# Performance work log

Hardware: AMD Instinct MI355X
Metric: run time of the kernel (lower is better)

The kernel has to match this reference:

```python
import jax, jax.numpy as jnp
import numpy as np

N = 50000      # nodes
E = 500000     # edges
D = 128        # in_dim == out_dim
L = 4          # encoder_layers
G = 64         # graphs in batch
FIXED = 10000  # fixed_input_dim
BN_EPS = 1e-5


def setup_inputs() -> dict:
    key = jax.random.key(0)
    ks = jax.random.split(key, 14)
    s = 0.05
    feat_id = jax.random.randint(ks[0], (N,), 0, FIXED)
    edge_index = jax.random.randint(ks[1], (2, E), 0, N)
    # sorted graph assignment guaranteeing all G graphs are non-empty
    batch = (jnp.arange(N) * G) // N
    return {
        "feat_id": feat_id,
        "edge_index": edge_index,
        "batch": batch,
        # value_projection: Linear(FIXED, D); store weight.T as a lookup table
        "value_proj_w": jax.random.normal(ks[2], (FIXED, D)) * s,
        "value_proj_b": jax.random.normal(ks[3], (D,)) * s,
        "deg_emb": jax.random.normal(ks[4], (1001, D)) * s,
        # stacked per-layer GIN MLP params: Linear -> BN -> ReLU -> Linear
        "mlp_w1": jax.random.normal(ks[5], (L, D, D)) * s,
        "mlp_b1": jax.random.normal(ks[6], (L, D)) * s,
        "bn1_g": 1.0 + 0.1 * jax.random.normal(ks[7], (L, D)),
        "bn1_b": 0.1 * jax.random.normal(ks[8], (L, D)),
        "mlp_w2": jax.random.normal(ks[9], (L, D, D)) * s,
        "mlp_b2": jax.random.normal(ks[10], (L, D)) * s,
        # outer per-layer BatchNorm1d
        "bn2_g": 1.0 + 0.1 * jax.random.normal(ks[11], (L, D)),
        "bn2_b": 0.1 * jax.random.normal(ks[12], (L, D)),
    }


def _bn(x, g, b):
    # BatchNorm1d in training mode: batch stats over the node axis, biased var
    mu = jnp.mean(x, axis=0)
    var = jnp.mean(jnp.square(x - mu), axis=0)
    return g * (x - mu) * jax.lax.rsqrt(var + BN_EPS) + b


def reference(feat_id, edge_index, batch, value_proj_w, value_proj_b, deg_emb,
              mlp_w1, mlp_b1, bn1_g, bn1_b, mlp_w2, mlp_b2, bn2_g, bn2_b):
    src, dst = edge_index[0], edge_index[1]
    # one_hot(feat_id % FIXED) @ W.T + b  ==  gather of transposed weight rows
    h_attr = value_proj_w[feat_id % FIXED] + value_proj_b  # [N, D]
    # in-degree embedding (clamped to [0, 1000])
    in_deg = jax.ops.segment_sum(jnp.ones((E,), jnp.int32), dst, num_segments=N)
    h = h_attr + deg_emb[jnp.clip(in_deg, 0, 1000)]
    for i in range(L):
        # GIN: sum_{j in N(v)} h_j + (1 + eps) * h_v, eps = 0 (learn_eps=False)
        agg = jax.ops.segment_sum(h[src], dst, num_segments=N) + h
        z = jax.nn.relu(_bn(agg @ mlp_w1[i] + mlp_b1[i], bn1_g[i], bn1_b[i]))
        z = z @ mlp_w2[i] + mlp_b2[i]
        h = jax.nn.relu(_bn(z, bn2_g[i], bn2_b[i]))
    # global mean pool per graph
    gsum = jax.ops.segment_sum(h, batch, num_segments=G)       # [G, D]
    cnt = jax.ops.segment_sum(jnp.ones((N, 1)), batch, num_segments=G)
    graph_feature = gsum / jnp.maximum(cnt, 1.0)
    return graph_feature, h
```

## Files before the change

### kernel.cpp

```cpp
#include <hip/hip_runtime.h>

#define NN 50000
#define NE 500000
#define DD 128
#define NL 4
#define NG 64
#define FIXED_DIM 10000
#define BN_EPS 1e-5f
#define NB 196

typedef unsigned short u16;
typedef unsigned int u32;
typedef __attribute__((ext_vector_type(8))) short bf16x8;
typedef __attribute__((ext_vector_type(4))) float f32x4;

__device__ __forceinline__ float bf2f(u16 u) {
    return __uint_as_float(((u32)u) << 16);
}
__device__ __forceinline__ u16 f2bf(float f) {
    u32 u = __float_as_uint(f);
    return (u16)((u + 0x7FFFu + ((u >> 16) & 1u)) >> 16);
}
__device__ __forceinline__ float ldf(const void* p, size_t i, int isbf) {
    return isbf ? bf2f(((const u16*)p)[i]) : ((const float*)p)[i];
}

__global__ void k_pre(const void* __restrict__ vb, int* __restrict__ flag,
                      const int* __restrict__ batch, int* __restrict__ goff,
                      float* __restrict__ zbase, int zwords) {
    int b = blockIdx.x, t = threadIdx.x;
    if (b == 0) {
        __shared__ int ok[256];
        float v = (t < 128) ? bf2f(((const u16*)vb)[t]) : 0.f;
        ok[t] = (t < 128) ? ((fabsf(v) < 1000.f) ? 1 : 0) : 1;
        __syncthreads();
        for (int off = 128; off; off >>= 1) {
            if (t < off) ok[t] &= ok[t + off];
            __syncthreads();
        }
        if (t == 0) *flag = ok[0];
    } else if (b == 1) {
        if (t <= NG) {
            int lo = 0, hi = NN;
            while (lo < hi) {
                int mid = (lo + hi) >> 1;
                if (batch[mid] < t) lo = mid + 1; else hi = mid;
            }
            goff[t] = lo;
        }
    } else {
        int i = (b - 2) * 256 + t;
        if (i < zwords) zbase[i] = 0.f;
    }
}

__global__ void k_cvtswz(const void* b1, const void* b2, const void* g1,
                         const void* be1, const void* g2, const void* be2,
                         const void* __restrict__ w1, const void* __restrict__ w2,
                         float* __restrict__ pc, u16* __restrict__ Wsw,
                         const int* __restrict__ flag) {
    int b = blockIdx.x, tt = threadIdx.x;
    if (b < 12) {
        int t = b * 256 + tt;
        int p = t >> 9, j = t & 511;
        const void* s = (p == 0) ? b1 : (p == 1) ? b2 : (p == 2) ? g1
                      : (p == 3) ? be1 : (p == 4) ? g2 : be2;
        pc[t] = ldf(s, j, *flag);
    } else {
        int t = (b - 12) * 256 + tt;
        int m    = t >> 14;
        int idx  = t & 16383;
        int nt   = idx >> 11;
        int ks   = (idx >> 9) & 3;
        int lane = (idx >> 3) & 63;
        int j    = idx & 7;
        int row = ks * 32 + (lane >> 4) * 8 + j;
        int col = nt * 16 + (lane & 15);
        const void* src = (m < 4) ? w1 : w2;
        size_t off = (size_t)(m & 3) * DD * DD + (size_t)row * DD + col;
        Wsw[t] = f2bf(ldf(src, off, *flag));
    }
}

__global__ void k_deg(const int* __restrict__ dst, int* __restrict__ deg) {
    int i = blockIdx.x * 256 + threadIdx.x;
    if (i < NE) atomicAdd(&deg[dst[i]], 1);
}

__global__ void k_scan12(const int* __restrict__ deg, int* __restrict__ bsum,
                         int* __restrict__ sem) {
    __shared__ int S[256];
    __shared__ int lastB;
    int b = blockIdx.x, t = threadIdx.x;
    int i = b * 256 + t;
    S[t] = (i < NN) ? deg[i] : 0;
    __syncthreads();
    for (int off = 128; off; off >>= 1) {
        if (t < off) S[t] += S[t + off];
        __syncthreads();
    }
    if (t == 0) {
        atomicExch(&bsum[b], S[0]);
        __threadfence();
        lastB = (atomicAdd(&sem[0], 1) == gridDim.x - 1);
    }
    __syncthreads();
    if (!lastB) return;
    __threadfence();
    int v = (t < NB) ? atomicAdd(&bsum[t], 0) : 0;
    S[t] = v;
    __syncthreads();
    for (int off = 1; off < 256; off <<= 1) {
        int x = (t >= off) ? S[t - off] : 0;
        __syncthreads();
        S[t] += x;
        __syncthreads();
    }
    if (t < NB) bsum[t] = S[t] - v;
}

__global__ void k_scan3init(const int* __restrict__ deg, const int* __restrict__ bsum,
                            int* __restrict__ rowptr,
                            const int* __restrict__ feat, const void* __restrict__ vw,
                            const void* __restrict__ vb, const void* __restrict__ demb,
                            u16* __restrict__ B, const int* __restrict__ flag) {
    __shared__ int S[256];
    int b = blockIdx.x, t = threadIdx.x;
    if (b < NB) {
        int i = b * 256 + t;
        int v = (i < NN) ? deg[i] : 0;
        S[t] = v;
        __syncthreads();
        for (int off = 1; off < 256; off <<= 1) {
            int x = (t >= off) ? S[t - off] : 0;
            __syncthreads();
            S[t] += x;
            __syncthreads();
        }
        if (i < NN) rowptr[i] = bsum[b] + S[t] - v;
        if (i == NN - 1) rowptr[NN] = bsum[b] + S[t];
    } else {
        int idx = (b - NB) * 256 + t;
        if (idx >= NN * DD) return;
        int n = idx >> 7, c = idx & 127;
        int isbf = *flag;
        int f = feat[n] % FIXED_DIM;
        int dg = min(deg[n], 1000);
        B[idx] = f2bf(ldf(vw, (size_t)f * DD + c, isbf)
                    + ldf(vb, c, isbf)
                    + ldf(demb, (size_t)dg * DD + c, isbf));
    }
}

__global__ void k_fill(const int* __restrict__ src, const int* __restrict__ dst,
                       const int* __restrict__ rowptr, int* __restrict__ cursor,
                       int* __restrict__ colidx) {
    int e = blockIdx.x * 256 + threadIdx.x;
    if (e >= NE) return;
    int d = dst[e];
    int p = atomicAdd(&cursor[d], 1);
    colidx[rowptr[d] + p] = src[e];
}

template <bool AFF>
__global__ __launch_bounds__(256, 8) void k_aggr(
        const u16* __restrict__ B, const int* __restrict__ rowptr,
        const int* __restrict__ colidx,
        const float* __restrict__ gIn, const float* __restrict__ bIn,
        const float* __restrict__ sIn, const float* __restrict__ qIn,
        u16* __restrict__ Agg) {
    int n = blockIdx.x * 4 + (threadIdx.x >> 6);
    if (n >= NN) return;
    int c = (threadIdx.x & 63) * 2;
    float a0 = 1.f, b0 = 0.f, a1 = 1.f, b1 = 0.f;
    if (AFF) {
        float inv = 1.0f / (float)NN;
        float mu0 = sIn[c] * inv, mu1 = sIn[c + 1] * inv;
        float v0 = fmaxf(qIn[c] * inv - mu0 * mu0, 0.f);
        float v1 = fmaxf(qIn[c + 1] * inv - mu1 * mu1, 0.f);
        a0 = gIn[c] * rsqrtf(v0 + BN_EPS);
        a1 = gIn[c + 1] * rsqrtf(v1 + BN_EPS);
        b0 = bIn[c] - a0 * mu0;
        b1 = bIn[c + 1] - a1 * mu1;
    }
    u32 w = *(const u32*)&B[(size_t)n * DD + c];
    float x0 = bf2f((u16)(w & 0xFFFF)), x1 = bf2f((u16)(w >> 16));
    float s0 = AFF ? fmaxf(fmaf(a0, x0, b0), 0.f) : x0;
    float s1 = AFF ? fmaxf(fmaf(a1, x1, b1), 0.f) : x1;
    int lo = rowptr[n], hi = rowptr[n + 1];
    int j = lo;
    for (; j + 4 <= hi; j += 4) {
        int m0 = colidx[j], m1 = colidx[j + 1];
        int m2 = colidx[j + 2], m3 = colidx[j + 3];
        u32 w0 = *(const u32*)&B[(size_t)m0 * DD + c];
        u32 w1v = *(const u32*)&B[(size_t)m1 * DD + c];
        u32 w2v = *(const u32*)&B[(size_t)m2 * DD + c];
        u32 w3v = *(const u32*)&B[(size_t)m3 * DD + c];
        float y;
        y = bf2f((u16)(w0 & 0xFFFF)); s0 += AFF ? fmaxf(fmaf(a0, y, b0), 0.f) : y;
        y = bf2f((u16)(w0 >> 16));    s1 += AFF ? fmaxf(fmaf(a1, y, b1), 0.f) : y;
        y = bf2f((u16)(w1v & 0xFFFF)); s0 += AFF ? fmaxf(fmaf(a0, y, b0), 0.f) : y;
        y = bf2f((u16)(w1v >> 16));    s1 += AFF ? fmaxf(fmaf(a1, y, b1), 0.f) : y;
        y = bf2f((u16)(w2v & 0xFFFF)); s0 += AFF ? fmaxf(fmaf(a0, y, b0), 0.f) : y;
        y = bf2f((u16)(w2v >> 16));    s1 += AFF ? fmaxf(fmaf(a1, y, b1), 0.f) : y;
        y = bf2f((u16)(w3v & 0xFFFF)); s0 += AFF ? fmaxf(fmaf(a0, y, b0), 0.f) : y;
        y = bf2f((u16)(w3v >> 16));    s1 += AFF ? fmaxf(fmaf(a1, y, b1), 0.f) : y;
    }
    for (; j < hi; j++) {
        int m = colidx[j];
        w = *(const u32*)&B[(size_t)m * DD + c];
        x0 = bf2f((u16)(w & 0xFFFF)); x1 = bf2f((u16)(w >> 16));
        s0 += AFF ? fmaxf(fmaf(a0, x0, b0), 0.f) : x0;
        s1 += AFF ? fmaxf(fmaf(a1, x1, b1), 0.f) : x1;
    }
    *(u32*)&Agg[(size_t)n * DD + c] = ((u32)f2bf(s1) << 16) | (u32)f2bf(s0);
}

template <bool IN16, bool OUT16, bool AFF>
__global__ __launch_bounds__(256, 2) void k_gemm(
        const void* In, const u16* __restrict__ Wsw,
        const float* __restrict__ bias,
        const float* __restrict__ gIn, const float* __restrict__ bIn,
        const float* __restrict__ sIn, const float* __restrict__ qIn,
        void* Out, float* __restrict__ ssum, float* __restrict__ ssq,
        int nRows) {
    __shared__ u16 Wl[16384];
    __shared__ u16 At[128 * 136];
    __shared__ float affS[256];
    float* RedS = (float*)At;
    float* RedQ = RedS + 512;
    const int t = threadIdx.x;
    const int row0 = blockIdx.x * 128;

    if (AFF) {
        if (t < 128) {
            float inv = 1.0f / (float)NN;
            float mu = sIn[t] * inv;
            float var = fmaxf(qIn[t] * inv - mu * mu, 0.f);
            float a = gIn[t] * rsqrtf(var + BN_EPS);
            affS[t] = a;
            affS[128 + t] = bIn[t] - a * mu;
        }
        __syncthreads();
    }

    {
        const uint4* s = (const uint4*)Wsw;
        uint4* d = (uint4*)Wl;
        #pragma unroll
        for (int i = 0; i < 8; i++) d[t + i * 256] = s[t + i * 256];
    }
    if (IN16) {
        for (int i = t; i < 2048; i += 256) {
            int r  = i >> 4;
            int c8 = (i & 15) * 8;
            int gr = row0 + r;
            uint4 v = make_uint4(0u, 0u, 0u, 0u);
            if (gr < nRows) v = *(const uint4*)&((const u16*)In)[(size_t)gr * DD + c8];
            *(uint4*)&At[r * 136 + c8] = v;
        }
    } else {
        for (int i = t; i < 4096; i += 256) {
            int r  = i >> 5;
            int c4 = (i & 31) * 4;
            int gr = row0 + r;
            float4 v = make_float4(0.f, 0.f, 0.f, 0.f);
            if (gr < nRows) {
                v = *(const float4*)&((const float*)In)[(size_t)gr * DD + c4];
                if (AFF) {
                    v.x = fmaxf(fmaf(affS[c4 + 0], v.x, affS[128 + c4 + 0]), 0.f);
                    v.y = fmaxf(fmaf(affS[c4 + 1], v.y, affS[128 + c4 + 1]), 0.f);
                    v.z = fmaxf(fmaf(affS[c4 + 2], v.z, affS[128 + c4 + 2]), 0.f);
                    v.w = fmaxf(fmaf(affS[c4 + 3], v.w, affS[128 + c4 + 3]), 0.f);
                }
            }
            ushort4 o;
            o.x = f2bf(v.x); o.y = f2bf(v.y); o.z = f2bf(v.z); o.w = f2bf(v.w);
            *(ushort4*)&At[r * 136 + c4] = o;
        }
    }
    __syncthreads();

    const int w    = t >> 6;
    const int ln   = t & 63;
    const int quad = ln >> 4;
    const int lq   = ln & 15;

    f32x4 acc0[8], acc1[8];
    #pragma unroll
    for (int nt = 0; nt < 8; nt++) {
        acc0[nt] = (f32x4){0.f, 0.f, 0.f, 0.f};
        acc1[nt] = (f32x4){0.f, 0.f, 0.f, 0.f};
    }

    const u16* aRow0 = &At[(w * 32 + lq) * 136 + quad * 8];
    const u16* aRow1 = &At[(w * 32 + 16 + lq) * 136 + quad * 8];
    #pragma unroll
    for (int ks = 0; ks < 4; ks++) {
        bf16x8 a0 = *(const bf16x8*)&aRow0[ks * 32];
        bf16x8 a1 = *(const bf16x8*)&aRow1[ks * 32];
        #pragma unroll
        for (int nt = 0; nt < 8; nt++) {
            bf16x8 b = *(const bf16x8*)&Wl[((nt * 4 + ks) * 64 + ln) * 8];
            acc0[nt] = __builtin_amdgcn_mfma_f32_16x16x32_bf16(a0, b, acc0[nt], 0, 0, 0);
            acc1[nt] = __builtin_amdgcn_mfma_f32_16x16x32_bf16(a1, b, acc1[nt], 0, 0, 0);
        }
    }
    __syncthreads();

    const int rb0 = row0 + w * 32 + quad * 4;
    const int rb1 = rb0 + 16;
    #pragma unroll
    for (int nt = 0; nt < 8; nt++) {
        int col = nt * 16 + lq;
        float bv = bias[col];
        float s = 0.f, q = 0.f;
        #pragma unroll
        for (int r = 0; r < 4; r++) {
            int gr = rb0 + r;
            if (gr < nRows) {
                float val = acc0[nt][r] + bv;
                size_t o = (size_t)gr * DD + col;
                if (OUT16) ((u16*)Out)[o] = f2bf(val);
                else       ((float*)Out)[o] = val;
                s += val; q += val * val;
            }
        }
        #pragma unroll
        for (int r = 0; r < 4; r++) {
            int gr = rb1 + r;
            if (gr < nRows) {
                float val = acc1[nt][r] + bv;
                size_t o = (size_t)gr * DD + col;
                if (OUT16) ((u16*)Out)[o] = f2bf(val);
                else       ((float*)Out)[o] = val;
                s += val; q += val * val;
            }
        }
        s += __shfl_xor(s, 16); q += __shfl_xor(q, 16);
        s += __shfl_xor(s, 32); q += __shfl_xor(q, 32);
        if (quad == 0) { RedS[w * 128 + col] = s; RedQ[w * 128 + col] = q; }
    }
    __syncthreads();
    if (t < 128) {
        float s = RedS[t] + RedS[128 + t] + RedS[256 + t] + RedS[384 + t];
        float q = RedQ[t] + RedQ[128 + t] + RedQ[256 + t] + RedQ[384 + t];
        atomicAdd(&ssum[t], s);
        atomicAdd(&ssq[t], q);
    }
}

__global__ __launch_bounds__(256, 4) void k_upool(
        const u16* __restrict__ Bz,
        const float* __restrict__ gIn, const float* __restrict__ bIn,
        const float* __restrict__ sIn, const float* __restrict__ qIn,
        const int* __restrict__ batch, float* __restrict__ A,
        float* __restrict__ gsum, const int* __restrict__ goff,
        float* __restrict__ outw, int* __restrict__ sem) {
    const int t = threadIdx.x;
    const int c = (t & 63) * 2;
    const int qv = t >> 6;
    const int r0 = blockIdx.x * 64;
    const int g_lo = batch[r0];
    const int g_hi = batch[min(r0 + 63, NN - 1)];
    float inv = 1.0f / (float)NN;
    float mu0 = sIn[c] * inv, mu1 = sIn[c + 1] * inv;
    float v0 = fmaxf(qIn[c] * inv - mu0 * mu0, 0.f);
    float v1 = fmaxf(qIn[c + 1] * inv - mu1 * mu1, 0.f);
    float a0 = gIn[c] * rsqrtf(v0 + BN_EPS);
    float a1 = gIn[c + 1] * rsqrtf(v1 + BN_EPS);
    float b0 = bIn[c] - a0 * mu0;
    float b1 = bIn[c + 1] - a1 * mu1;
    float lo0 = 0.f, lo1 = 0.f, hi0 = 0.f, hi1 = 0.f;
    #pragma unroll
    for (int i = 0; i < 16; i++) {
        int r = r0 + qv + 4 * i;
        if (r >= NN) break;
        u32 wd = *(const u32*)&Bz[(size_t)r * DD + c];
        float x0 = fmaxf(fmaf(a0, bf2f((u16)(wd & 0xFFFF)), b0), 0.f);
        float x1 = fmaxf(fmaf(a1, bf2f((u16)(wd >> 16)), b1), 0.f);
        *(float2*)&A[(size_t)r * DD + c] = make_float2(x0, x1);
        if (batch[r] == g_lo) { lo0 += x0; lo1 += x1; }
        else                  { hi0 += x0; hi1 += x1; }
    }
    __shared__ float2 PL[4][64];
    __shared__ float2 PH[4][64];
    PL[qv][t & 63] = make_float2(lo0, lo1);
    PH[qv][t & 63] = make_float2(hi0, hi1);
    __syncthreads();
    if (t < 64) {
        float2 p0 = PL[0][t], p1 = PL[1][t], p2 = PL[2][t], p3 = PL[3][t];
        atomicAdd(&gsum[(size_t)g_lo * DD + 2 * t],     p0.x + p1.x + p2.x + p3.x);
        atomicAdd(&gsum[(size_t)g_lo * DD + 2 * t + 1], p0.y + p1.y + p2.y + p3.y);
    } else if (t < 128 && g_hi != g_lo) {
        int u = t - 64;
        float2 p0 = PH[0][u], p1 = PH[1][u], p2 = PH[2][u], p3 = PH[3][u];
        atomicAdd(&gsum[(size_t)g_hi * DD + 2 * u],     p0.x + p1.x + p2.x + p3.x);
        atomicAdd(&gsum[(size_t)g_hi * DD + 2 * u + 1], p0.y + p1.y + p2.y + p3.y);
    }

    __shared__ int lastF;
    if (t == 0) {
        __threadfence();
        lastF = (atomicAdd(&sem[1], 1) == gridDim.x - 1);
    }
    __syncthreads();
    if (!lastF) return;
    __threadfence();
    for (int i = t; i < NG * DD; i += 256) {
        int g = i >> 7;
        float cnt = fmaxf((float)(goff[g + 1] - goff[g]), 1.0f);
        outw[i] = atomicAdd(&gsum[i], 0.0f) / cnt;
    }
}

extern "C" void kernel_launch(void* const* d_in, const int* in_sizes, int n_in,
                              void* d_out, int out_size, void* d_ws, size_t ws_size,
                              hipStream_t stream) {
    const int* feat  = (const int*)d_in[0];
    const int* ei    = (const int*)d_in[1];
    const int* batch = (const int*)d_in[2];
    const void* vw   = d_in[3];
    const void* vb   = d_in[4];
    const void* demb = d_in[5];
    const void* w1   = d_in[6];
    const void* b1   = d_in[7];
    const void* g1   = d_in[8];
    const void* be1  = d_in[9];
    const void* w2   = d_in[10];
    const void* b2   = d_in[11];
    const void* g2   = d_in[12];
    const void* be2  = d_in[13];

    const int* src = ei;
    const int* dst = ei + NE;
    const size_t ND = (size_t)NN * DD;

    float* pc     = (float*)d_ws;
    int*   flag   = (int*)(pc + 3072);
    float* stats  = (float*)(flag + 64);
    float* gsum   = stats + 2048;
    int*   deg    = (int*)(gsum + 8192);
    int*   cursor = deg + NN;
    int*   sem    = cursor + NN;
    int*   bsum   = sem + 64;
    int*   goff   = bsum + 256;
    int*   rowptr = goff + 128;
    int*   colidx = rowptr + NN + 64;
    u16*   Wsw    = (u16*)(colidx + NE);
    u16*   B      = Wsw + 8 * 16384;
    u16*   Agg16  = B + ND;

    float* b1c  = pc;
    float* b2c  = pc + 512;
    float* g1c  = pc + 1024;
    float* be1c = pc + 1536;
    float* g2c  = pc + 2048;
    float* be2c = pc + 2560;
    float* sum1 = stats;
    float* sq1  = stats + 512;
    float* sum2 = stats + 1024;
    float* sq2  = stats + 1536;

    float* outw = (float*)d_out;
    float* A    = outw + (size_t)NG * DD;

    const int zwords = 2048 + 8192 + NN + NN + 64;
    const int gridND = (int)(ND / 256);
    const int gemmBlocks = (NN + 127) / 128;
    const int aggrBlocks = (NN + 3) / 4;

    k_pre<<<2 + (zwords + 255) / 256, 256, 0, stream>>>(vb, flag, batch, goff,
                                                        stats, zwords);
    k_cvtswz<<<12 + 512, 256, 0, stream>>>(b1, b2, g1, be1, g2, be2, w1, w2,
                                           pc, Wsw, flag);
    k_deg<<<(NE + 255) / 256, 256, 0, stream>>>(dst, deg);
    k_scan12<<<NB, 256, 0, stream>>>(deg, bsum, sem);
    k_scan3init<<<NB + gridND, 256, 0, stream>>>(deg, bsum, rowptr,
                                                 feat, vw, vb, demb, B, flag);
    k_fill<<<(NE + 255) / 256, 256, 0, stream>>>(src, dst, rowptr, cursor, colidx);

    for (int l = 0; l < NL; l++) {
        const u16* W1l = Wsw + (size_t)l * 16384;
        const u16* W2l = Wsw + (size_t)(4 + l) * 16384;
        if (l == 0) {
            k_aggr<false><<<aggrBlocks, 256, 0, stream>>>(
                B, rowptr, colidx, nullptr, nullptr, nullptr, nullptr, Agg16);
        } else {
            k_aggr<true><<<aggrBlocks, 256, 0, stream>>>(
                B, rowptr, colidx, g2c + (l - 1) * 128, be2c + (l - 1) * 128,
                sum2 + (l - 1) * 128, sq2 + (l - 1) * 128, Agg16);
        }
        k_gemm<true, false, false><<<gemmBlocks, 256, 0, stream>>>(
            Agg16, W1l, b1c + l * 128, nullptr, nullptr, nullptr, nullptr,
            A, sum1 + l * 128, sq1 + l * 128, NN);
        k_gemm<false, true, true><<<gemmBlocks, 256, 0, stream>>>(
            A, W2l, b2c + l * 128, g1c + l * 128, be1c + l * 128,
            sum1 + l * 128, sq1 + l * 128,
            B, sum2 + l * 128, sq2 + l * 128, NN);
    }
    k_upool<<<(NN + 63) / 64, 256, 0, stream>>>(
        B, g2c + 3 * 128, be2c + 3 * 128, sum2 + 3 * 128, sq2 + 3 * 128,
        batch, A, gsum, goff, outw, sem);
}
```

Before: 548.4 us.

## Fuse both GIN MLP GEMMs into one kernel with grid barrier for BN stats

Merges the two per-layer GEMM kernels into a single persistent kernel. The first GEMM's output stays in registers, a software grid-wide barrier on a semaphore waits for the global BN1 statistics, then BN+ReLU is applied in place and the second GEMM runs from LDS. This avoids writing and re-reading the fp32 intermediate activation and saves one launch per layer. The cost is a spin barrier that needs every block (391 at 2 per CU) to be co-resident, which risks deadlock if they are not, plus idle time while blocks wait.

Result: slower. 654.3 us (+19.3%).

```diff
diff --git a/kernel.cpp b/kernel.cpp
--- a/kernel.cpp
+++ b/kernel.cpp
@@ -216,14 +216,15 @@
     *(u32*)&Agg[(size_t)n * DD + c] = ((u32)f2bf(s1) << 16) | (u32)f2bf(s0);
 }
 
-template <bool IN16, bool OUT16, bool AFF>
-__global__ __launch_bounds__(256, 2) void k_gemm(
-        const void* In, const u16* __restrict__ Wsw,
-        const float* __restrict__ bias,
-        const float* __restrict__ gIn, const float* __restrict__ bIn,
-        const float* __restrict__ sIn, const float* __restrict__ qIn,
-        void* Out, float* __restrict__ ssum, float* __restrict__ ssq,
-        int nRows) {
+__global__ __launch_bounds__(256, 2) void k_mlp(
+        const u16* __restrict__ Agg,
+        const u16* __restrict__ W1sw, const u16* __restrict__ W2sw,
+        const float* __restrict__ bias1, const float* __restrict__ bias2,
+        const float* __restrict__ g1v, const float* __restrict__ be1v,
+        float* __restrict__ sum1, float* __restrict__ sq1,
+        u16* __restrict__ OutB,
+        float* __restrict__ sum2, float* __restrict__ sq2,
+        int* __restrict__ sem) {
     __shared__ u16 Wl[16384];
     __shared__ u16 At[128 * 136];
     __shared__ float affS[256];
@@ -232,52 +233,19 @@
     const int t = threadIdx.x;
     const int row0 = blockIdx.x * 128;
 
-    if (AFF) {
-        if (t < 128) {
-            float inv = 1.0f / (float)NN;
-            float mu = sIn[t] * inv;
-            float var = fmaxf(qIn[t] * inv - mu * mu, 0.f);
-            float a = gIn[t] * rsqrtf(var + BN_EPS);
-            affS[t] = a;
-            affS[128 + t] = bIn[t] - a * mu;
-        }
-        __syncthreads();
-    }
-
     {
-        const uint4* s = (const uint4*)Wsw;
+        const uint4* s = (const uint4*)W1sw;
         uint4* d = (uint4*)Wl;
         #pragma unroll
         for (int i = 0; i < 8; i++) d[t + i * 256] = s[t + i * 256];
     }
-    if (IN16) {
-        for (int i = t; i < 2048; i += 256) {
-            int r  = i >> 4;
-            int c8 = (i & 15) * 8;
-            int gr = row0 + r;
-            uint4 v = make_uint4(0u, 0u, 0u, 0u);
-            if (gr < nRows) v = *(const uint4*)&((const u16*)In)[(size_t)gr * DD + c8];
-            *(uint4*)&At[r * 136 + c8] = v;
-        }
-    } else {
-        for (int i = t; i < 4096; i += 256) {
-            int r  = i >> 5;
-            int c4 = (i & 31) * 4;
-            int gr = row0 + r;
-            float4 v = make_float4(0.f, 0.f, 0.f, 0.f);
-            if (gr < nRows) {
-                v = *(const float4*)&((const float*)In)[(size_t)gr * DD + c4];
-                if (AFF) {
-                    v.x = fmaxf(fmaf(affS[c4 + 0], v.x, affS[128 + c4 + 0]), 0.f);
-                    v.y = fmaxf(fmaf(affS[c4 + 1], v.y, affS[128 + c4 + 1]), 0.f);
-                    v.z = fmaxf(fmaf(affS[c4 + 2], v.z, affS[128 + c4 + 2]), 0.f);
-                    v.w = fmaxf(fmaf(affS[c4 + 3], v.w, affS[128 + c4 + 3]), 0.f);
-                }
-            }
-            ushort4 o;
-            o.x = f2bf(v.x); o.y = f2bf(v.y); o.z = f2bf(v.z); o.w = f2bf(v.w);
-            *(ushort4*)&At[r * 136 + c4] = o;
-        }
+    for (int i = t; i < 2048; i += 256) {
+        int r  = i >> 4;
+        int c8 = (i & 15) * 8;
+        int gr = row0 + r;
+        uint4 v = make_uint4(0u, 0u, 0u, 0u);
+        if (gr < NN) v = *(const uint4*)&Agg[(size_t)gr * DD + c8];
+        *(uint4*)&At[r * 136 + c8] = v;
     }
     __syncthreads();
 
@@ -292,51 +260,43 @@
         acc0[nt] = (f32x4){0.f, 0.f, 0.f, 0.f};
         acc1[nt] = (f32x4){0.f, 0.f, 0.f, 0.f};
     }
-
-    const u16* aRow0 = &At[(w * 32 + lq) * 136 + quad * 8];
-    const u16* aRow1 = &At[(w * 32 + 16 + lq) * 136 + quad * 8];
-    #pragma unroll
-    for (int ks = 0; ks < 4; ks++) {
-        bf16x8 a0 = *(const bf16x8*)&aRow0[ks * 32];
-        bf16x8 a1 = *(const bf16x8*)&aRow1[ks * 32];
-        #pragma unroll
-        for (int nt = 0; nt < 8; nt++) {
-            bf16x8 b = *(const bf16x8*)&Wl[((nt * 4 + ks) * 64 + ln) * 8];
-            acc0[nt] = __builtin_amdgcn_mfma_f32_16x16x32_bf16(a0, b, acc0[nt], 0, 0, 0);
-            acc1[nt] = __builtin_amdgcn_mfma_f32_16x16x32_bf16(a1, b, acc1[nt], 0, 0, 0);
-        }
-    }
-    __syncthreads();
+    {
+        const u16* aRow0 = &At[(w * 32 + lq) * 136 + quad * 8];
+        const u16* aRow1 = &At[(w * 32 + 16 + lq) * 136 + quad * 8];
+        #pragma unroll
+        for (int ks = 0; ks < 4; ks++) {
+            bf16x8 a0 = *(const bf16x8*)&aRow0[ks * 32];
+            bf16x8 a1 = *(const bf16x8*)&aRow1[ks * 32];
+            #pragma unroll
+            for (int nt = 0; nt < 8; nt++) {
+                bf16x8 b = *(const bf16x8*)&Wl[((nt * 4 + ks) * 64 + ln) * 8];
+                acc0[nt] = __builtin_amdgcn_mfma_f32_16x16x32_bf16(a0, b, acc0[nt], 0, 0, 0);
+                acc1[nt] = __builtin_amdgcn_mfma_f32_16x16x32_bf16(a1, b, acc1[nt], 0, 0, 0);
+            }
+        }
+    }
+    __syncthreads();
+
+    {
+        const uint4* s = (const uint4*)W2sw;
+        uint4* d = (uint4*)Wl;
+        #pragma unroll
+        for (int i = 0; i < 8; i++) d[t + i * 256] = s[t + i * 256];
+    }
 
     const int rb0 = row0 + w * 32 + quad * 4;
     const int rb1 = rb0 + 16;
     #pragma unroll
     for (int nt = 0; nt < 8; nt++) {
         int col = nt * 16 + lq;
-        float bv = bias[col];
+        float bv = bias1[col];
         float s = 0.f, q = 0.f;
         #pragma unroll
-        for (int r = 0; r < 4; r++) {
-            int gr = rb0 + r;
-            if (gr < nRows) {
-                float val = acc0[nt][r] + bv;
-                size_t o = (size_t)gr * DD + col;
-                if (OUT16) ((u16*)Out)[o] = f2bf(val);
-                else       ((float*)Out)[o] = val;
-                s += val; q += val * val;
-            }
-        }
-        #pragma unroll
-        for (int r = 0; r < 4; r++) {
-            int gr = rb1 + r;
-            if (gr < nRows) {
-                float val = acc1[nt][r] + bv;
-                size_t o = (size_t)gr * DD + col;
-                if (OUT16) ((u16*)Out)[o] = f2bf(val);
-                else       ((float*)Out)[o] = val;
-                s += val; q += val * val;
-            }
-        }
+        for (int r = 0; r < 4; r++)
+            if (rb0 + r < NN) { float v = acc0[nt][r] + bv; s += v; q += v * v; }
+        #pragma unroll
+        for (int r = 0; r < 4; r++)
+            if (rb1 + r < NN) { float v = acc1[nt][r] + bv; s += v; q += v * v; }
         s += __shfl_xor(s, 16); q += __shfl_xor(q, 16);
         s += __shfl_xor(s, 32); q += __shfl_xor(q, 32);
         if (quad == 0) { RedS[w * 128 + col] = s; RedQ[w * 128 + col] = q; }
@@ -345,8 +305,112 @@
     if (t < 128) {
         float s = RedS[t] + RedS[128 + t] + RedS[256 + t] + RedS[384 + t];
         float q = RedQ[t] + RedQ[128 + t] + RedQ[256 + t] + RedQ[384 + t];
-        atomicAdd(&ssum[t], s);
-        atomicAdd(&ssq[t], q);
+        atomicAdd(&sum1[t], s);
+        atomicAdd(&sq1[t], q);
+    }
+    __syncthreads();
+
+    if (t == 0) {
+        __threadfence();
+        atomicAdd(sem, 1);
+        while (__hip_atomic_load(sem, __ATOMIC_RELAXED, __HIP_MEMORY_SCOPE_AGENT)
+               < (int)gridDim.x)
+            __builtin_amdgcn_s_sleep(8);
+    }
+    __syncthreads();
+    __threadfence();
+
+    if (t < 128) {
+        float sv = __hip_atomic_load(&sum1[t], __ATOMIC_RELAXED, __HIP_MEMORY_SCOPE_AGENT);
+        float qv = __hip_atomic_load(&sq1[t],  __ATOMIC_RELAXED, __HIP_MEMORY_SCOPE_AGENT);
+        float inv = 1.0f / (float)NN;
+        float mu = sv * inv;
+        float var = fmaxf(qv * inv - mu * mu, 0.f);
+        float a = g1v[t] * rsqrtf(var + BN_EPS);
+        affS[t] = a;
+        affS[128 + t] = be1v[t] - a * mu;
+    }
+    __syncthreads();
+
+    #pragma unroll
+    for (int nt = 0; nt < 8; nt++) {
+        int col = nt * 16 + lq;
+        float bv = bias1[col];
+        float a = affS[col], bb = affS[128 + col];
+        #pragma unroll
+        for (int r = 0; r < 4; r++) {
+            int lr = w * 32 + quad * 4 + r;
+            u16 ov = 0;
+            if (row0 + lr < NN)
+                ov = f2bf(fmaxf(fmaf(a, acc0[nt][r] + bv, bb), 0.f));
+            At[lr * 136 + col] = ov;
+        }
+        #pragma unroll
+        for (int r = 0; r < 4; r++) {
+            int lr = w * 32 + 16 + quad * 4 + r;
+            u16 ov = 0;
+            if (row0 + lr < NN)
+                ov = f2bf(fmaxf(fmaf(a, acc1[nt][r] + bv, bb), 0.f));
+            At[lr * 136 + col] = ov;
+        }
+    }
+    __syncthreads();
+
+    #pragma unroll
+    for (int nt = 0; nt < 8; nt++) {
+        acc0[nt] = (f32x4){0.f, 0.f, 0.f, 0.f};
+        acc1[nt] = (f32x4){0.f, 0.f, 0.f, 0.f};
+    }
+    {
+        const u16* aRow0 = &At[(w * 32 + lq) * 136 + quad * 8];
+        const u16* aRow1 = &At[(w * 32 + 16 + lq) * 136 + quad * 8];
+        #pragma unroll
+        for (int ks = 0; ks < 4; ks++) {
+            bf16x8 a0 = *(const bf16x8*)&aRow0[ks * 32];
+            bf16x8 a1 = *(const bf16x8*)&aRow1[ks * 32];
+            #pragma unroll
+            for (int nt = 0; nt < 8; nt++) {
+                bf16x8 b = *(const bf16x8*)&Wl[((nt * 4 + ks) * 64 + ln) * 8];
+                acc0[nt] = __builtin_amdgcn_mfma_f32_16x16x32_bf16(a0, b, acc0[nt], 0, 0, 0);
+                acc1[nt] = __builtin_amdgcn_mfma_f32_16x16x32_bf16(a1, b, acc1[nt], 0, 0, 0);
+            }
+        }
+    }
+    __syncthreads();
+
+    #pragma unroll
+    for (int nt = 0; nt < 8; nt++) {
+        int col = nt * 16 + lq;
+        float bv = bias2[col];
+        float s = 0.f, q = 0.f;
+        #pragma unroll
+        for (int r = 0; r < 4; r++) {
+            int gr = rb0 + r;
+            if (gr < NN) {
+                float val = acc0[nt][r] + bv;
+                OutB[(size_t)gr * DD + col] = f2bf(val);
+                s += val; q += val * val;
+            }
+        }
+        #pragma unroll
+        for (int r = 0; r < 4; r++) {
+            int gr = rb1 + r;
+            if (gr < NN) {
+                float val = acc1[nt][r] + bv;
+                OutB[(size_t)gr * DD + col] = f2bf(val);
+                s += val; q += val * val;
+            }
+        }
+        s += __shfl_xor(s, 16); q += __shfl_xor(q, 16);
+        s += __shfl_xor(s, 32); q += __shfl_xor(q, 32);
+        if (quad == 0) { RedS[w * 128 + col] = s; RedQ[w * 128 + col] = q; }
+    }
+    __syncthreads();
+    if (t < 128) {
+        float s = RedS[t] + RedS[128 + t] + RedS[256 + t] + RedS[384 + t];
+        float q = RedQ[t] + RedQ[128 + t] + RedQ[256 + t] + RedQ[384 + t];
+        atomicAdd(&sum2[t], s);
+        atomicAdd(&sq2[t], q);
     }
 }
 
@@ -491,13 +555,12 @@
                 B, rowptr, colidx, g2c + (l - 1) * 128, be2c + (l - 1) * 128,
                 sum2 + (l - 1) * 128, sq2 + (l - 1) * 128, Agg16);
         }
-        k_gemm<true, false, false><<<gemmBlocks, 256, 0, stream>>>(
-            Agg16, W1l, b1c + l * 128, nullptr, nullptr, nullptr, nullptr,
-            A, sum1 + l * 128, sq1 + l * 128, NN);
-        k_gemm<false, true, true><<<gemmBlocks, 256, 0, stream>>>(
-            A, W2l, b2c + l * 128, g1c + l * 128, be1c + l * 128,
+        k_mlp<<<gemmBlocks, 256, 0, stream>>>(
+            Agg16, W1l, W2l, b1c + l * 128, b2c + l * 128,
+            g1c + l * 128, be1c + l * 128,
             sum1 + l * 128, sq1 + l * 128,
-            B, sum2 + l * 128, sq2 + l * 128, NN);
+            B, sum2 + l * 128, sq2 + l * 128,
+            sem + 2 + l);
     }
     k_upool<<<(NN + 63) / 64, 256, 0, stream>>>(
         B, g2c + 3 * 128, be2c + 3 * 128, sum2 + 3 * 128, sq2 + 3 * 128,
```

## Load GEMM A-fragments directly from global memory and vectorize init embedding

Applied to the files above, without the earlier changes.

The GEMM kernel no longer stages the activation tile in LDS. Each wave loads its MFMA A-fragments straight from global memory into registers, applying the BN affine and bf16 conversion there, which removes the LDS round trip and a barrier. The smaller LDS footprint lets launch bounds rise to 3 blocks per CU, at the cost of more registers and less coalesced global loads. The init embedding kernel also processes 8 channels per thread with 128-bit loads and stores.

Result: faster. 527.0 us (-3.9%).

```diff
diff --git a/kernel.cpp b/kernel.cpp
--- a/kernel.cpp
+++ b/kernel.cpp
@@ -141,14 +141,38 @@
         if (i == NN - 1) rowptr[NN] = bsum[b] + S[t];
     } else {
         int idx = (b - NB) * 256 + t;
-        if (idx >= NN * DD) return;
-        int n = idx >> 7, c = idx & 127;
+        if (idx >= NN * DD / 8) return;
+        int n  = idx >> 4;
+        int c8 = (idx & 15) * 8;
         int isbf = *flag;
-        int f = feat[n] % FIXED_DIM;
+        int f  = feat[n] % FIXED_DIM;
         int dg = min(deg[n], 1000);
-        B[idx] = f2bf(ldf(vw, (size_t)f * DD + c, isbf)
-                    + ldf(vb, c, isbf)
-                    + ldf(demb, (size_t)dg * DD + c, isbf));
+        float x[8];
+        if (isbf) {
+            uint4 a4 = *(const uint4*)((const u16*)vw + (size_t)f * DD + c8);
+            uint4 b4 = *(const uint4*)((const u16*)vb + c8);
+            uint4 d4 = *(const uint4*)((const u16*)demb + (size_t)dg * DD + c8);
+            u32 aw[4] = {a4.x, a4.y, a4.z, a4.w};
+            u32 bw[4] = {b4.x, b4.y, b4.z, b4.w};
+            u32 dw[4] = {d4.x, d4.y, d4.z, d4.w};
+            #pragma unroll
+            for (int e = 0; e < 8; e++) {
+                int wi = e >> 1, sh = (e & 1) * 16;
+                x[e] = bf2f((u16)(aw[wi] >> sh)) + bf2f((u16)(bw[wi] >> sh))
+                     + bf2f((u16)(dw[wi] >> sh));
+            }
+        } else {
+            const float* vwp = (const float*)vw + (size_t)f * DD + c8;
+            const float* vbp = (const float*)vb + c8;
+            const float* dep = (const float*)demb + (size_t)dg * DD + c8;
+            #pragma unroll
+            for (int e = 0; e < 8; e++) x[e] = vwp[e] + vbp[e] + dep[e];
+        }
+        u32 o0 = ((u32)f2bf(x[1]) << 16) | (u32)f2bf(x[0]);
+        u32 o1 = ((u32)f2bf(x[3]) << 16) | (u32)f2bf(x[2]);
+        u32 o2 = ((u32)f2bf(x[5]) << 16) | (u32)f2bf(x[4]);
+        u32 o3 = ((u32)f2bf(x[7]) << 16) | (u32)f2bf(x[6]);
+        *(uint4*)&B[(size_t)idx * 8] = make_uint4(o0, o1, o2, o3);
     }
 }
 
@@ -217,7 +241,7 @@
 }
 
 template <bool IN16, bool OUT16, bool AFF>
-__global__ __launch_bounds__(256, 2) void k_gemm(
+__global__ __launch_bounds__(256, 3) void k_gemm(
         const void* In, const u16* __restrict__ Wsw,
         const float* __restrict__ bias,
         const float* __restrict__ gIn, const float* __restrict__ bIn,
@@ -225,24 +249,11 @@
         void* Out, float* __restrict__ ssum, float* __restrict__ ssq,
         int nRows) {
     __shared__ u16 Wl[16384];
-    __shared__ u16 At[128 * 136];
+    __shared__ float RedS[512];
+    __shared__ float RedQ[512];
     __shared__ float affS[256];
-    float* RedS = (float*)At;
-    float* RedQ = RedS + 512;
     const int t = threadIdx.x;
     const int row0 = blockIdx.x * 128;
-
-    if (AFF) {
-        if (t < 128) {
-            float inv = 1.0f / (float)NN;
-            float mu = sIn[t] * inv;
-            float var = fmaxf(qIn[t] * inv - mu * mu, 0.f);
-            float a = gIn[t] * rsqrtf(var + BN_EPS);
-            affS[t] = a;
-            affS[128 + t] = bIn[t] - a * mu;
-        }
-        __syncthreads();
-    }
 
     {
         const uint4* s = (const uint4*)Wsw;
@@ -250,34 +261,13 @@
         #pragma unroll
         for (int i = 0; i < 8; i++) d[t + i * 256] = s[t + i * 256];
     }
-    if (IN16) {
-        for (int i = t; i < 2048; i += 256) {
-            int r  = i >> 4;
-            int c8 = (i & 15) * 8;
-            int gr = row0 + r;
-            uint4 v = make_uint4(0u, 0u, 0u, 0u);
-            if (gr < nRows) v = *(const uint4*)&((const u16*)In)[(size_t)gr * DD + c8];
-            *(uint4*)&At[r * 136 + c8] = v;
-        }
-    } else {
-        for (int i = t; i < 4096; i += 256) {
-            int r  = i >> 5;
-            int c4 = (i & 31) * 4;
-            int gr = row0 + r;
-            float4 v = make_float4(0.f, 0.f, 0.f, 0.f);
-            if (gr < nRows) {
-                v = *(const float4*)&((const float*)In)[(size_t)gr * DD + c4];
-                if (AFF) {
-                    v.x = fmaxf(fmaf(affS[c4 + 0], v.x, affS[128 + c4 + 0]), 0.f);
-                    v.y = fmaxf(fmaf(affS[c4 + 1], v.y, affS[128 + c4 + 1]), 0.f);
-                    v.z = fmaxf(fmaf(affS[c4 + 2], v.z, affS[128 + c4 + 2]), 0.f);
-                    v.w = fmaxf(fmaf(affS[c4 + 3], v.w, affS[128 + c4 + 3]), 0.f);
-                }
-            }
-            ushort4 o;
-            o.x = f2bf(v.x); o.y = f2bf(v.y); o.z = f2bf(v.z); o.w = f2bf(v.w);
-            *(ushort4*)&At[r * 136 + c4] = o;
-        }
+    if (AFF && t < 128) {
+        float inv = 1.0f / (float)NN;
+        float mu = sIn[t] * inv;
+        float var = fmaxf(qIn[t] * inv - mu * mu, 0.f);
+        float a = gIn[t] * rsqrtf(var + BN_EPS);
+        affS[t] = a;
+        affS[128 + t] = bIn[t] - a * mu;
     }
     __syncthreads();
 
@@ -285,6 +275,50 @@
     const int ln   = t & 63;
     const int quad = ln >> 4;
     const int lq   = ln & 15;
+    const int r0g  = row0 + w * 32 + lq;
+    const int r1g  = r0g + 16;
+
+    bf16x8 af0[4], af1[4];
+    #pragma unroll
+    for (int ks = 0; ks < 4; ks++) {
+        const int cb = quad * 8 + ks * 32;
+        if (IN16) {
+            const u16* p = (const u16*)In;
+            af0[ks] = (r0g < nRows) ? *(const bf16x8*)&p[(size_t)r0g * DD + cb]
+                                    : (bf16x8){0,0,0,0,0,0,0,0};
+            af1[ks] = (r1g < nRows) ? *(const bf16x8*)&p[(size_t)r1g * DD + cb]
+                                    : (bf16x8){0,0,0,0,0,0,0,0};
+        } else {
+            const float* p = (const float*)In;
+            bf16x8 v0 = {0,0,0,0,0,0,0,0}, v1 = {0,0,0,0,0,0,0,0};
+            if (r0g < nRows) {
+                const float* rp = p + (size_t)r0g * DD + cb;
+                float4 lo = *(const float4*)rp;
+                float4 hi = *(const float4*)(rp + 4);
+                float xs[8] = {lo.x, lo.y, lo.z, lo.w, hi.x, hi.y, hi.z, hi.w};
+                #pragma unroll
+                for (int e = 0; e < 8; e++) {
+                    float x = xs[e];
+                    if (AFF) x = fmaxf(fmaf(affS[cb + e], x, affS[128 + cb + e]), 0.f);
+                    v0[e] = (short)f2bf(x);
+                }
+            }
+            if (r1g < nRows) {
+                const float* rp = p + (size_t)r1g * DD + cb;
+                float4 lo = *(const float4*)rp;
+                float4 hi = *(const float4*)(rp + 4);
+                float xs[8] = {lo.x, lo.y, lo.z, lo.w, hi.x, hi.y, hi.z, hi.w};
+                #pragma unroll
+                for (int e = 0; e < 8; e++) {
+                    float x = xs[e];
+                    if (AFF) x = fmaxf(fmaf(affS[cb + e], x, affS[128 + cb + e]), 0.f);
+                    v1[e] = (short)f2bf(x);
+                }
+            }
+            af0[ks] = v0;
+            af1[ks] = v1;
+        }
+    }
 
     f32x4 acc0[8], acc1[8];
     #pragma unroll
@@ -292,21 +326,15 @@
         acc0[nt] = (f32x4){0.f, 0.f, 0.f, 0.f};
         acc1[nt] = (f32x4){0.f, 0.f, 0.f, 0.f};
     }
-
-    const u16* aRow0 = &At[(w * 32 + lq) * 136 + quad * 8];
-    const u16* aRow1 = &At[(w * 32 + 16 + lq) * 136 + quad * 8];
     #pragma unroll
     for (int ks = 0; ks < 4; ks++) {
-        bf16x8 a0 = *(const bf16x8*)&aRow0[ks * 32];
-        bf16x8 a1 = *(const bf16x8*)&aRow1[ks * 32];
         #pragma unroll
         for (int nt = 0; nt < 8; nt++) {
             bf16x8 b = *(const bf16x8*)&Wl[((nt * 4 + ks) * 64 + ln) * 8];
-            acc0[nt] = __builtin_amdgcn_mfma_f32_16x16x32_bf16(a0, b, acc0[nt], 0, 0, 0);
-            acc1[nt] = __builtin_amdgcn_mfma_f32_16x16x32_bf16(a1, b, acc1[nt], 0, 0, 0);
-        }
-    }
-    __syncthreads();
+            acc0[nt] = __builtin_amdgcn_mfma_f32_16x16x32_bf16(af0[ks], b, acc0[nt], 0, 0, 0);
+            acc1[nt] = __builtin_amdgcn_mfma_f32_16x16x32_bf16(af1[ks], b, acc1[nt], 0, 0, 0);
+        }
+    }
 
     const int rb0 = row0 + w * 32 + quad * 4;
     const int rb1 = rb0 + 16;
@@ -466,7 +494,7 @@
     float* A    = outw + (size_t)NG * DD;
 
     const int zwords = 2048 + 8192 + NN + NN + 64;
-    const int gridND = (int)(ND / 256);
+    const int initBlocks = (int)(ND / 8 / 256);
     const int gemmBlocks = (NN + 127) / 128;
     const int aggrBlocks = (NN + 3) / 4;
 
@@ -476,8 +504,8 @@
                                            pc, Wsw, flag);
     k_deg<<<(NE + 255) / 256, 256, 0, stream>>>(dst, deg);
     k_scan12<<<NB, 256, 0, stream>>>(deg, bsum, sem);
-    k_scan3init<<<NB + gridND, 256, 0, stream>>>(deg, bsum, rowptr,
-                                                 feat, vw, vb, demb, B, flag);
+    k_scan3init<<<NB + initBlocks, 256, 0, stream>>>(deg, bsum, rowptr,
+                                                     feat, vw, vb, demb, B, flag);
     k_fill<<<(NE + 255) / 256, 256, 0, stream>>>(src, dst, rowptr, cursor, colidx);
 
     for (int l = 0; l < NL; l++) {
```
